# Kernel optimization log

Hardware: AMD Instinct MI355X
Metric: run time of the kernel (lower is better)

Reference implementation:

```python
import jax, jax.numpy as jnp
import numpy as np

IMG = 32        # imgSize
NU = 96         # n_units per grid axis
SHAPE = IMG * NU
ALPHA = 0.9     # running_variance_alpha
EPS_LR = 1e-07


def setup_inputs() -> dict:
    key = jax.random.key(0)
    k1, k2 = jax.random.split(key)
    x = jax.random.uniform(k1, (IMG, IMG), dtype=jnp.float32)
    som = jnp.clip(0.1 + 0.3 * jax.random.normal(k2, (SHAPE, SHAPE), dtype=jnp.float32), 0.0, 1.0)
    running_variance = jnp.ones((SHAPE, SHAPE), jnp.float32)
    radius = 48.0 * jnp.ones((NU, NU), jnp.float32)
    learning_rates = 0.5 * jnp.ones((NU, NU), jnp.float32)
    bmu_count = jnp.zeros((NU, NU, 10), jnp.float32)
    return {"x": x, "som": som, "running_variance": running_variance,
            "radius": radius, "learning_rates": learning_rates, "bmu_count": bmu_count}


def reference(x, som, running_variance, radius, learning_rates, bmu_count):
    # --- layer1: variance-weighted squared distance of input to every unit tile ---
    som_b = som.reshape(NU, IMG, NU, IMG).transpose(0, 2, 1, 3)            # [NU,NU,IMG,IMG]
    var_b = running_variance.reshape(NU, IMG, NU, IMG).transpose(0, 2, 1, 3)
    diff = som_b - x                                                        # broadcast input over grid
    z = jnp.sum(diff * diff / var_b, axis=(2, 3))                           # [NU,NU] feature map
    # --- layer2: BMU = argmin over the unit grid ---
    flat = jnp.argmin(z)
    bi = flat // NU
    bj = flat % NU
    input_matrix = jnp.tile(x, (NU, NU))                                    # [SHAPE,SHAPE]
    # --- create_mask: neighborhood-weighted codebook + EMA variance update ---
    r = radius[bi, bj]
    lr_b = learning_rates[bi, bj]
    dm = 1.0 / (2.0 * r * r)                                                # distance_modifier
    constant = -jnp.log(EPS_LR / lr_b) / dm
    ii = jnp.arange(NU, dtype=jnp.float32)
    bif = bi.astype(jnp.float32)
    bjf = bj.astype(jnp.float32)
    cart = jnp.sqrt((ii[:, None] - bif) ** 2 + (ii[None, :] - bjf) ** 2)    # cartesian_distances[:,:,bi,bj]
    modifier = jnp.where(cart > r, 0.0, cart)
    fm = learning_rates * jnp.exp(-modifier) * dm                           # [NU,NU]
    fm_full = jnp.repeat(jnp.repeat(fm, IMG, axis=1), IMG, axis=0)          # [SHAPE,SHAPE]
    va = jnp.clip(ALPHA - 0.5 + jax.nn.sigmoid(cart / constant), 0.0, 1.0)
    va_full = jnp.repeat(jnp.repeat(va, IMG, axis=1), IMG, axis=0)
    new_som = som + fm_full * (input_matrix - som)
    new_var = va_full * running_variance + (1.0 - va_full) * (input_matrix - new_som) ** 2
    new_som = jnp.clip(new_som, 0.0, 1.0)
    # --- decayRadius / decayLearningRate at the BMU (per-class counts -> class 0 used) ---
    new_radius = jnp.maximum(radius.at[bi, bj].set(jnp.exp(-bmu_count[bi, bj, 0] / 15.0)), 1e-05)
    new_lr = jnp.maximum(learning_rates.at[bi, bj].set(jnp.exp(-bmu_count[bi, bj, 0] / 25.0)), 1e-05)
    return new_som, new_var, new_radius, new_lr
```

## Files before the change

kernel.cpp:

```cpp
#include <hip/hip_runtime.h>
#include <math.h>

#define NU 96
#define IMG 32
#define SHAPE (NU * IMG)
#define NUNITS (NU * NU)
#define PLANE (SHAPE * SHAPE)
#define SHAPE4 (SHAPE / 4)
#define IMG4 (IMG / 4)

__global__ __launch_bounds__(256) void zkernel(const float* __restrict__ x,
                                               const float* __restrict__ som,
                                               const float* __restrict__ var,
                                               float* __restrict__ z) {
    const int v = blockIdx.x, u = blockIdx.y, t = threadIdx.x;
    const int i = t >> 3;
    const int jv = t & 7;

    const float4* __restrict__ som4 = (const float4*)som;
    const float4* __restrict__ var4 = (const float4*)var;
    const float4* __restrict__ x4   = (const float4*)x;

    const int idx = (u * IMG + i) * SHAPE4 + v * IMG4 + jv;
    const float4 s  = som4[idx];
    const float4 w  = var4[idx];
    const float4 xx = x4[i * IMG4 + jv];

    const float d0 = s.x - xx.x, d1 = s.y - xx.y, d2 = s.z - xx.z, d3 = s.w - xx.w;
    float p = d0 * d0 / w.x + d1 * d1 / w.y + d2 * d2 / w.z + d3 * d3 / w.w;

    #pragma unroll
    for (int off = 32; off > 0; off >>= 1) p += __shfl_down(p, off, 64);

    __shared__ float lds[4];
    const int wave = t >> 6, lane = t & 63;
    if (lane == 0) lds[wave] = p;
    __syncthreads();
    if (t == 0) z[u * NU + v] = lds[0] + lds[1] + lds[2] + lds[3];
}

__global__ __launch_bounds__(256) void argmin_kernel(const float* __restrict__ z,
                                                     int* __restrict__ bmu) {
    const int t = threadIdx.x;
    float mv = 3.402823466e38f;
    int mi = 0x7fffffff;
    for (int k = t; k < NUNITS; k += 256) {
        const float val = z[k];
        if (val < mv || (val == mv && k < mi)) { mv = val; mi = k; }
    }
    #pragma unroll
    for (int off = 32; off > 0; off >>= 1) {
        const float ov = __shfl_down(mv, off, 64);
        const int   oi = __shfl_down(mi, off, 64);
        if (ov < mv || (ov == mv && oi < mi)) { mv = ov; mi = oi; }
    }
    __shared__ float svals[4];
    __shared__ int   sidx[4];
    const int wave = t >> 6, lane = t & 63;
    if (lane == 0) { svals[wave] = mv; sidx[wave] = mi; }
    __syncthreads();
    if (t == 0) {
        #pragma unroll
        for (int w = 1; w < 4; w++) {
            if (svals[w] < mv || (svals[w] == mv && sidx[w] < mi)) { mv = svals[w]; mi = sidx[w]; }
        }
        bmu[0] = mi;
    }
}

__global__ __launch_bounds__(256) void update_kernel(const float* __restrict__ x,
                                                     const float* __restrict__ som,
                                                     const float* __restrict__ var,
                                                     const float* __restrict__ radius,
                                                     const float* __restrict__ lrates,
                                                     const float* __restrict__ bmu_count,
                                                     const int* __restrict__ bmu,
                                                     float* __restrict__ out) {
    const int v = blockIdx.x, u = blockIdx.y, t = threadIdx.x;
    const int flat = bmu[0];
    const int bi = flat / NU, bj = flat % NU;

    const float r    = radius[flat];
    const float lr_b = lrates[flat];
    const float dm   = 1.0f / (2.0f * r * r);
    const float constant = -logf(1e-7f / lr_b) / dm;

    const float du = (float)u - (float)bi;
    const float dv = (float)v - (float)bj;
    const float cart = sqrtf(du * du + dv * dv);
    const float modifier = (cart > r) ? 0.0f : cart;
    const float fm = lrates[u * NU + v] * expf(-modifier) * dm;
    const float sg = 1.0f / (1.0f + expf(-(cart / constant)));
    float va = 0.4f + sg;
    va = fminf(fmaxf(va, 0.0f), 1.0f);
    const float one_minus_va = 1.0f - va;

    const float4* __restrict__ som4 = (const float4*)som;
    const float4* __restrict__ var4 = (const float4*)var;
    const float4* __restrict__ x4   = (const float4*)x;
    float4* __restrict__ out_som = (float4*)out;
    float4* __restrict__ out_var = (float4*)(out + (size_t)PLANE);

    const int i = t >> 3, jv = t & 7;
    const int idx = (u * IMG + i) * SHAPE4 + v * IMG4 + jv;
    const float4 s  = som4[idx];
    const float4 w  = var4[idx];
    const float4 xx = x4[i * IMG4 + jv];

    float4 ns, nv;
    {
        float n = s.x + fm * (xx.x - s.x);
        float d = xx.x - n;
        nv.x = va * w.x + one_minus_va * d * d;
        ns.x = fminf(fmaxf(n, 0.0f), 1.0f);
    }
    {
        float n = s.y + fm * (xx.y - s.y);
        float d = xx.y - n;
        nv.y = va * w.y + one_minus_va * d * d;
        ns.y = fminf(fmaxf(n, 0.0f), 1.0f);
    }
    {
        float n = s.z + fm * (xx.z - s.z);
        float d = xx.z - n;
        nv.z = va * w.z + one_minus_va * d * d;
        ns.z = fminf(fmaxf(n, 0.0f), 1.0f);
    }
    {
        float n = s.w + fm * (xx.w - s.w);
        float d = xx.w - n;
        nv.w = va * w.w + one_minus_va * d * d;
        ns.w = fminf(fmaxf(n, 0.0f), 1.0f);
    }
    out_som[idx] = ns;
    out_var[idx] = nv;

    if (t == 0) {
        float* out_rad = out + 2 * (size_t)PLANE;
        float* out_lr  = out_rad + NUNITS;
        const int uv = u * NU + v;
        const float b0 = bmu_count[(size_t)flat * 10];
        const float rv = (uv == flat) ? expf(-b0 / 15.0f) : radius[uv];
        const float lv = (uv == flat) ? expf(-b0 / 25.0f) : lrates[uv];
        out_rad[uv] = fmaxf(rv, 1e-5f);
        out_lr[uv]  = fmaxf(lv, 1e-5f);
    }
}

extern "C" void kernel_launch(void* const* d_in, const int* in_sizes, int n_in,
                              void* d_out, int out_size, void* d_ws, size_t ws_size,
                              hipStream_t stream) {
    const float* x         = (const float*)d_in[0];
    const float* som       = (const float*)d_in[1];
    const float* var       = (const float*)d_in[2];
    const float* radius    = (const float*)d_in[3];
    const float* lrates    = (const float*)d_in[4];
    const float* bmu_count = (const float*)d_in[5];
    float* out = (float*)d_out;

    float* z  = (float*)d_ws;
    int* bmu  = (int*)((float*)d_ws + NUNITS);

    dim3 grid(NU, NU);
    zkernel<<<grid, 256, 0, stream>>>(x, som, var, z);
    argmin_kernel<<<1, 256, 0, stream>>>(z, bmu);
    update_kernel<<<grid, 256, 0, stream>>>(x, som, var, radius, lrates, bmu_count, bmu, out);
}
```

Before: 167.6 us.

## Fuse argmin into distance kernel via 64-bit atomicMin slots

Removes the separate single-block argmin kernel. Each distance block now packs its float score and flat index into a 64-bit key and atomicMins it into one of 64 slots, which are cleared by a memset. The update kernel reduces the 64 slots with a wave shuffle to recover the BMU. Elementwise math moves to ext_vector_type, and outputs use nontemporal stores. This trades a kernel launch and a serial reduction for atomics, a memset, and a redundant per-block slot reduction.

```diff
diff --git a/kernel.cpp b/kernel.cpp
--- a/kernel.cpp
+++ b/kernel.cpp
@@ -8,26 +8,30 @@
 #define PLANE (SHAPE * SHAPE)
 #define SHAPE4 (SHAPE / 4)
 #define IMG4 (IMG / 4)
+#define NSLOTS 64
 
-__global__ __launch_bounds__(256) void zkernel(const float* __restrict__ x,
-                                               const float* __restrict__ som,
-                                               const float* __restrict__ var,
-                                               float* __restrict__ z) {
+typedef float vfloat4 __attribute__((ext_vector_type(4)));
+
+__global__ __launch_bounds__(256) void zargmin_kernel(const float* __restrict__ x,
+                                                      const float* __restrict__ som,
+                                                      const float* __restrict__ var,
+                                                      unsigned long long* __restrict__ slots) {
     const int v = blockIdx.x, u = blockIdx.y, t = threadIdx.x;
     const int i = t >> 3;
     const int jv = t & 7;
 
-    const float4* __restrict__ som4 = (const float4*)som;
-    const float4* __restrict__ var4 = (const float4*)var;
-    const float4* __restrict__ x4   = (const float4*)x;
+    const vfloat4* __restrict__ som4 = (const vfloat4*)som;
+    const vfloat4* __restrict__ var4 = (const vfloat4*)var;
+    const vfloat4* __restrict__ x4   = (const vfloat4*)x;
 
     const int idx = (u * IMG + i) * SHAPE4 + v * IMG4 + jv;
-    const float4 s  = som4[idx];
-    const float4 w  = var4[idx];
-    const float4 xx = x4[i * IMG4 + jv];
+    const vfloat4 s  = som4[idx];
+    const vfloat4 w  = var4[idx];
+    const vfloat4 xx = x4[i * IMG4 + jv];
 
-    const float d0 = s.x - xx.x, d1 = s.y - xx.y, d2 = s.z - xx.z, d3 = s.w - xx.w;
-    float p = d0 * d0 / w.x + d1 * d1 / w.y + d2 * d2 / w.z + d3 * d3 / w.w;
+    const vfloat4 d = s - xx;
+    const vfloat4 q = d * d / w;
+    float p = q.x + q.y + q.z + q.w;
 
     #pragma unroll
     for (int off = 32; off > 0; off >>= 1) p += __shfl_down(p, off, 64);
@@ -36,35 +40,12 @@
     const int wave = t >> 6, lane = t & 63;
     if (lane == 0) lds[wave] = p;
     __syncthreads();
-    if (t == 0) z[u * NU + v] = lds[0] + lds[1] + lds[2] + lds[3];
-}
-
-__global__ __launch_bounds__(256) void argmin_kernel(const float* __restrict__ z,
-                                                     int* __restrict__ bmu) {
-    const int t = threadIdx.x;
-    float mv = 3.402823466e38f;
-    int mi = 0x7fffffff;
-    for (int k = t; k < NUNITS; k += 256) {
-        const float val = z[k];
-        if (val < mv || (val == mv && k < mi)) { mv = val; mi = k; }
-    }
-    #pragma unroll
-    for (int off = 32; off > 0; off >>= 1) {
-        const float ov = __shfl_down(mv, off, 64);
-        const int   oi = __shfl_down(mi, off, 64);
-        if (ov < mv || (ov == mv && oi < mi)) { mv = ov; mi = oi; }
-    }
-    __shared__ float svals[4];
-    __shared__ int   sidx[4];
-    const int wave = t >> 6, lane = t & 63;
-    if (lane == 0) { svals[wave] = mv; sidx[wave] = mi; }
-    __syncthreads();
     if (t == 0) {
-        #pragma unroll
-        for (int w = 1; w < 4; w++) {
-            if (svals[w] < mv || (svals[w] == mv && sidx[w] < mi)) { mv = svals[w]; mi = sidx[w]; }
-        }
-        bmu[0] = mi;
+        const float z = lds[0] + lds[1] + lds[2] + lds[3];
+        const unsigned int flat = (unsigned int)(u * NU + v);
+        const unsigned long long key =
+            ((unsigned long long)__float_as_uint(z) << 32) | (unsigned long long)flat;
+        atomicMin(&slots[flat & (NSLOTS - 1)], key);
     }
 }
 
@@ -74,10 +55,17 @@
                                                      const float* __restrict__ radius,
                                                      const float* __restrict__ lrates,
                                                      const float* __restrict__ bmu_count,
-                                                     const int* __restrict__ bmu,
+                                                     const unsigned long long* __restrict__ slots,
                                                      float* __restrict__ out) {
     const int v = blockIdx.x, u = blockIdx.y, t = threadIdx.x;
-    const int flat = bmu[0];
+
+    unsigned long long key = slots[t & 63];
+    #pragma unroll
+    for (int off = 32; off > 0; off >>= 1) {
+        const unsigned long long o = __shfl_xor(key, off, 64);
+        key = (o < key) ? o : key;
+    }
+    const int flat = (int)(key & 0xFFFFFFFFull);
     const int bi = flat / NU, bj = flat % NU;
 
     const float r    = radius[flat];
@@ -95,45 +83,29 @@
     va = fminf(fmaxf(va, 0.0f), 1.0f);
     const float one_minus_va = 1.0f - va;
 
-    const float4* __restrict__ som4 = (const float4*)som;
-    const float4* __restrict__ var4 = (const float4*)var;
-    const float4* __restrict__ x4   = (const float4*)x;
-    float4* __restrict__ out_som = (float4*)out;
-    float4* __restrict__ out_var = (float4*)(out + (size_t)PLANE);
+    const vfloat4* __restrict__ som4 = (const vfloat4*)som;
+    const vfloat4* __restrict__ var4 = (const vfloat4*)var;
+    const vfloat4* __restrict__ x4   = (const vfloat4*)x;
+    vfloat4* __restrict__ out_som = (vfloat4*)out;
+    vfloat4* __restrict__ out_var = (vfloat4*)(out + (size_t)PLANE);
 
     const int i = t >> 3, jv = t & 7;
     const int idx = (u * IMG + i) * SHAPE4 + v * IMG4 + jv;
-    const float4 s  = som4[idx];
-    const float4 w  = var4[idx];
-    const float4 xx = x4[i * IMG4 + jv];
+    const vfloat4 s  = som4[idx];
+    const vfloat4 w  = var4[idx];
+    const vfloat4 xx = x4[i * IMG4 + jv];
 
-    float4 ns, nv;
-    {
-        float n = s.x + fm * (xx.x - s.x);
-        float d = xx.x - n;
-        nv.x = va * w.x + one_minus_va * d * d;
-        ns.x = fminf(fmaxf(n, 0.0f), 1.0f);
-    }
-    {
-        float n = s.y + fm * (xx.y - s.y);
-        float d = xx.y - n;
-        nv.y = va * w.y + one_minus_va * d * d;
-        ns.y = fminf(fmaxf(n, 0.0f), 1.0f);
-    }
-    {
-        float n = s.z + fm * (xx.z - s.z);
-        float d = xx.z - n;
-        nv.z = va * w.z + one_minus_va * d * d;
-        ns.z = fminf(fmaxf(n, 0.0f), 1.0f);
-    }
-    {
-        float n = s.w + fm * (xx.w - s.w);
-        float d = xx.w - n;
-        nv.w = va * w.w + one_minus_va * d * d;
-        ns.w = fminf(fmaxf(n, 0.0f), 1.0f);
-    }
-    out_som[idx] = ns;
-    out_var[idx] = nv;
+    const vfloat4 n = s + fm * (xx - s);
+    const vfloat4 d = xx - n;
+    const vfloat4 nv = va * w + one_minus_va * d * d;
+    vfloat4 ns;
+    ns.x = fminf(fmaxf(n.x, 0.0f), 1.0f);
+    ns.y = fminf(fmaxf(n.y, 0.0f), 1.0f);
+    ns.z = fminf(fmaxf(n.z, 0.0f), 1.0f);
+    ns.w = fminf(fmaxf(n.w, 0.0f), 1.0f);
+
+    __builtin_nontemporal_store(ns, &out_som[idx]);
+    __builtin_nontemporal_store(nv, &out_var[idx]);
 
     if (t == 0) {
         float* out_rad = out + 2 * (size_t)PLANE;
@@ -158,11 +130,11 @@
     const float* bmu_count = (const float*)d_in[5];
     float* out = (float*)d_out;
 
-    float* z  = (float*)d_ws;
-    int* bmu  = (int*)((float*)d_ws + NUNITS);
+    unsigned long long* slots = (unsigned long long*)d_ws;
+
+    (void)hipMemsetAsync(slots, 0xFF, NSLOTS * sizeof(unsigned long long), stream);
 
     dim3 grid(NU, NU);
-    zkernel<<<grid, 256, 0, stream>>>(x, som, var, z);
-    argmin_kernel<<<1, 256, 0, stream>>>(z, bmu);
-    update_kernel<<<grid, 256, 0, stream>>>(x, som, var, radius, lrates, bmu_count, bmu, out);
+    zargmin_kernel<<<grid, 256, 0, stream>>>(x, som, var, slots);
+    update_kernel<<<grid, 256, 0, stream>>>(x, som, var, radius, lrates, bmu_count, slots, out);
 }
```

Result: faster. 159.8 us (-4.7%).
